# Kernel tuning notes

Hardware: AMD Instinct MI355X
Metric: run time of the kernel (lower is better)

Reference implementation:

```python
import jax, jax.numpy as jnp
import numpy as np


def setup_inputs() -> dict:
    key = jax.random.key(0)
    k1, k2 = jax.random.split(key)
    B, C, H, W = 4, 64, 256, 512
    l_fmap = jax.random.normal(k1, (B, C, H, W), dtype=jnp.float32)
    r_fmap = jax.random.normal(k2, (B, C, H, W), dtype=jnp.float32)
    return {"l_fmap": l_fmap, "r_fmap": r_fmap, "max_disp": 48}


def reference(l_fmap, r_fmap, max_disp):
    # l_fmap, r_fmap: [B, C, H, W]
    w = l_fmap.shape[-1]
    # zero-pad right fmap along width by max_disp on both sides
    r_pad = jnp.pad(r_fmap, ((0, 0), (0, 0), (0, 0), (max_disp, max_disp)))
    planes = []
    for d in range(-max_disp, max_disp + 1):  # fixed small loop over 2*max_disp+1 disparities
        begin = max_disp - d
        # channel-mean of elementwise correlation at shift d -> [B, H, W]
        planes.append(jnp.mean(l_fmap * r_pad[:, :, :, begin:begin + w], axis=1))
    # cost volume: [B, 2*max_disp+1, H, W]
    return jnp.stack(planes, axis=1)
```

## Files before the change

kernel.cpp:

```cpp
#include <hip/hip_runtime.h>


#define B_  4
#define C_  64
#define H_  256
#define W_  512
#define ND  97
#define HW  (H_ * W_)

#define WBLK 256
#define RCOL 352
#define PADH 257
#define CH0  49

typedef __attribute__((ext_vector_type(8))) short  short8;
typedef __attribute__((ext_vector_type(4))) float  floatx4;

__device__ __forceinline__ unsigned f2bf(float f) {
    unsigned u = __builtin_bit_cast(unsigned, f);
    return (u + 0x7FFFu + ((u >> 16) & 1u)) >> 16;
}

union SM {
    struct {
        short l[WBLK * C_];
        short r[RCOL * C_];
    } st;
    float out_s[CH0 * PADH];
};

__global__ __launch_bounds__(512, 4) void cost_volume_kernel(
    const float* __restrict__ L, const float* __restrict__ R,
    float* __restrict__ out)
{
    __shared__ SM sm;
    const int tid  = threadIdx.x;
    const int half = blockIdx.x;
    const int h    = blockIdx.y;
    const int b    = blockIdx.z;
    const int w0   = half << 8;
    const size_t in_base = (((size_t)b * C_) * H_ + h) * (size_t)W_;

    {
        const int wl = tid & 255;
        const int ch = tid >> 8;
        const int m  = wl & 15, wq = wl >> 4;
        const float* lp = L + in_base + w0 + wl;
        const float* rp = R + in_base + w0 + wl;
        #pragma unroll
        for (int i = 0; i < 4; ++i) {
            const int cc = ch + 2 * i;
            unsigned dl[4], dr[4];
            #pragma unroll
            for (int jj = 0; jj < 4; ++jj) {
                float l0 = lp[(size_t)(cc * 8 + 2 * jj)     * HW] * 0.015625f;
                float l1 = lp[(size_t)(cc * 8 + 2 * jj + 1) * HW] * 0.015625f;
                float r0 = rp[(size_t)(cc * 8 + 2 * jj)     * HW];
                float r1 = rp[(size_t)(cc * 8 + 2 * jj + 1) * HW];
                dl[jj] = f2bf(l0) | (f2bf(l1) << 16);
                dr[jj] = f2bf(r0) | (f2bf(r1) << 16);
            }
            const int lchunk = ( wq      * 8 + cc) * 16 + m;
            const int rchunk = ((wq + 3) * 8 + cc) * 16 + m;
            *((uint4*)&sm.st.l[lchunk * 8]) = make_uint4(dl[0], dl[1], dl[2], dl[3]);
            *((uint4*)&sm.st.r[rchunk * 8]) = make_uint4(dr[0], dr[1], dr[2], dr[3]);
        }
    }
    if (tid < 192) {
        const int ch = tid & 1;
        const int hl = tid >> 1;
        const int ul = (hl < 48) ? hl : hl + 256;
        const int u  = w0 - 48 + ul;
        const bool valid = (unsigned)u < (unsigned)W_;
        const int m = ul & 15, uq = ul >> 4;
        const float* rp = R + in_base + (valid ? u : 0);
        #pragma unroll
        for (int i = 0; i < 4; ++i) {
            const int cc = ch + 2 * i;
            unsigned dr[4];
            #pragma unroll
            for (int jj = 0; jj < 4; ++jj) {
                float r0 = rp[(size_t)(cc * 8 + 2 * jj)     * HW];
                float r1 = rp[(size_t)(cc * 8 + 2 * jj + 1) * HW];
                r0 = valid ? r0 : 0.f;
                r1 = valid ? r1 : 0.f;
                dr[jj] = f2bf(r0) | (f2bf(r1) << 16);
            }
            const int rchunk = (uq * 8 + cc) * 16 + m;
            *((uint4*)&sm.st.r[rchunk * 8]) = make_uint4(dr[0], dr[1], dr[2], dr[3]);
        }
    }
    __syncthreads();

    const int lane = tid & 63;
    const int wv   = tid >> 6;
    const int q    = lane >> 4, m16 = lane & 15;
    const short8* lv = (const short8*)sm.st.l;
    const short8* rv = (const short8*)sm.st.r;

    floatx4 acc[2][7];
    #pragma unroll
    for (int hf = 0; hf < 2; ++hf) {
        const int lt = wv + 8 * hf;
        const short8 a0 = lv[(lt * 8 +     q) * 16 + m16];
        const short8 a1 = lv[(lt * 8 + 4 + q) * 16 + m16];
        #pragma unroll
        for (int t = 0; t < 7; ++t) {
            const int ut = lt + t;
            floatx4 c = {0.f, 0.f, 0.f, 0.f};
            const short8 b0 = rv[(ut * 8 +     q) * 16 + m16];
            const short8 b1 = rv[(ut * 8 + 4 + q) * 16 + m16];
            c = __builtin_amdgcn_mfma_f32_16x16x32_bf16(a0, b0, c, 0, 0, 0);
            c = __builtin_amdgcn_mfma_f32_16x16x32_bf16(a1, b1, c, 0, 0, 0);
            acc[hf][t] = c;
        }
    }

    float* ob = out + (((size_t)b * ND) * H_ + h) * (size_t)W_ + w0;
    int lo = 0;
    #pragma unroll
    for (int ck = 0; ck < 2; ++ck) {
        const int cnt = ck ? (ND - CH0) : CH0;
        __syncthreads();
        #pragma unroll
        for (int hf = 0; hf < 2; ++hf) {
            const int lt = wv + 8 * hf;
            #pragma unroll
            for (int t = 0; t < 7; ++t) {
                #pragma unroll
                for (int r = 0; r < 4; ++r) {
                    const int ml    = q * 4 + r;
                    const int d_idx = ml - m16 + 96 - 16 * t;
                    const int drel  = d_idx - lo;
                    if ((unsigned)drel < (unsigned)cnt)
                        sm.out_s[drel * PADH + lt * 16 + ml] = acc[hf][t][r];
                }
            }
        }
        __syncthreads();
        for (int i = tid; i < cnt * WBLK; i += 512) {
            const int pr = i >> 8, w = i & 255;
            ob[(size_t)(lo + pr) * HW + w] = sm.out_s[pr * PADH + w];
        }
        lo += CH0;
    }
}

extern "C" void kernel_launch(void* const* d_in, const int* in_sizes, int n_in,
                              void* d_out, int out_size, void* d_ws, size_t ws_size,
                              hipStream_t stream) {
    const float* L = (const float*)d_in[0];
    const float* R = (const float*)d_in[1];
    float* out = (float*)d_out;
    (void)in_sizes; (void)n_in; (void)d_ws; (void)ws_size; (void)out_size;
    dim3 grid(2, H_, B_);
    hipLaunchKernelGGL(cost_volume_kernel, grid, dim3(512), 0, stream, L, R, out);
}
```

Before: 394.2 us.

## Make cost-volume kernel persistent with register-prefetched next-row loads

```diff
diff --git a/kernel.cpp b/kernel.cpp
--- a/kernel.cpp
+++ b/kernel.cpp
@@ -12,6 +12,8 @@
 #define RCOL 352
 #define PADH 257
 #define CH0  49
+#define NBLK 256
+#define NROW 8
 
 typedef __attribute__((ext_vector_type(8))) short  short8;
 typedef __attribute__((ext_vector_type(4))) float  floatx4;
@@ -21,128 +23,159 @@
     return (u + 0x7FFFu + ((u >> 16) & 1u)) >> 16;
 }
 
-union SM {
-    struct {
-        short l[WBLK * C_];
-        short r[RCOL * C_];
-    } st;
+struct SM {
+    short l[WBLK * C_];
+    short r[RCOL * C_];
     float out_s[CH0 * PADH];
 };
 
-__global__ __launch_bounds__(512, 4) void cost_volume_kernel(
+__global__ __launch_bounds__(512, 2) void cost_volume_kernel(
     const float* __restrict__ L, const float* __restrict__ R,
     float* __restrict__ out)
 {
     __shared__ SM sm;
     const int tid  = threadIdx.x;
-    const int half = blockIdx.x;
-    const int h    = blockIdx.y;
-    const int b    = blockIdx.z;
+    const int bid  = blockIdx.x;
+    const int half = bid & 1;
+    const int hb   = bid >> 1;
     const int w0   = half << 8;
-    const size_t in_base = (((size_t)b * C_) * H_ + h) * (size_t)W_;
 
-    {
-        const int wl = tid & 255;
-        const int ch = tid >> 8;
-        const int m  = wl & 15, wq = wl >> 4;
-        const float* lp = L + in_base + w0 + wl;
-        const float* rp = R + in_base + w0 + wl;
+    const int wl = tid & 255;
+    const int ch = tid >> 8;
+    const int m  = wl & 15, wq = wl >> 4;
+
+    const bool hhalo = tid < 384;
+    const int hcol = tid % 96;
+    const int hch  = tid / 96;
+    const int hul  = (hcol < 48) ? hcol : hcol + 256;
+    const int hu   = w0 - 48 + hul;
+    const bool hvalid = hhalo && ((unsigned)hu < (unsigned)W_);
+
+    float Lf[32], Rf[32], Hf[16];
+
+    auto issue = [&](int k) {
+        const int b = k >> 1;
+        const int h = hb + ((k & 1) << 7);
+        const size_t base = ((size_t)b * C_ * H_ + h) * (size_t)W_;
+        const float* lp = L + base + w0 + wl;
+        const float* rp = R + base + w0 + wl;
+        #pragma unroll
+        for (int i = 0; i < 4; ++i) {
+            const int cc = ch + 2 * i;
+            #pragma unroll
+            for (int jj = 0; jj < 8; ++jj) {
+                Lf[i * 8 + jj] = lp[(size_t)(cc * 8 + jj) * HW];
+                Rf[i * 8 + jj] = rp[(size_t)(cc * 8 + jj) * HW];
+            }
+        }
+        if (hhalo) {
+            const float* hp = R + base + (hvalid ? hu : (w0 + wl));
+            #pragma unroll
+            for (int kk = 0; kk < 16; ++kk)
+                Hf[kk] = hp[(size_t)(hch * 16 + kk) * HW];
+        }
+    };
+
+    auto commit = [&]() {
         #pragma unroll
         for (int i = 0; i < 4; ++i) {
             const int cc = ch + 2 * i;
             unsigned dl[4], dr[4];
             #pragma unroll
             for (int jj = 0; jj < 4; ++jj) {
-                float l0 = lp[(size_t)(cc * 8 + 2 * jj)     * HW] * 0.015625f;
-                float l1 = lp[(size_t)(cc * 8 + 2 * jj + 1) * HW] * 0.015625f;
-                float r0 = rp[(size_t)(cc * 8 + 2 * jj)     * HW];
-                float r1 = rp[(size_t)(cc * 8 + 2 * jj + 1) * HW];
-                dl[jj] = f2bf(l0) | (f2bf(l1) << 16);
-                dr[jj] = f2bf(r0) | (f2bf(r1) << 16);
+                dl[jj] = f2bf(Lf[i * 8 + 2 * jj]     * 0.015625f)
+                       | (f2bf(Lf[i * 8 + 2 * jj + 1] * 0.015625f) << 16);
+                dr[jj] = f2bf(Rf[i * 8 + 2 * jj])
+                       | (f2bf(Rf[i * 8 + 2 * jj + 1]) << 16);
             }
-            const int lchunk = ( wq      * 8 + cc) * 16 + m;
-            const int rchunk = ((wq + 3) * 8 + cc) * 16 + m;
-            *((uint4*)&sm.st.l[lchunk * 8]) = make_uint4(dl[0], dl[1], dl[2], dl[3]);
-            *((uint4*)&sm.st.r[rchunk * 8]) = make_uint4(dr[0], dr[1], dr[2], dr[3]);
+            *((uint4*)&sm.l[(( wq      * 8 + cc) * 16 + m) * 8]) =
+                make_uint4(dl[0], dl[1], dl[2], dl[3]);
+            *((uint4*)&sm.r[(((wq + 3) * 8 + cc) * 16 + m) * 8]) =
+                make_uint4(dr[0], dr[1], dr[2], dr[3]);
         }
-    }
-    if (tid < 192) {
-        const int ch = tid & 1;
-        const int hl = tid >> 1;
-        const int ul = (hl < 48) ? hl : hl + 256;
-        const int u  = w0 - 48 + ul;
-        const bool valid = (unsigned)u < (unsigned)W_;
-        const int m = ul & 15, uq = ul >> 4;
-        const float* rp = R + in_base + (valid ? u : 0);
-        #pragma unroll
-        for (int i = 0; i < 4; ++i) {
-            const int cc = ch + 2 * i;
-            unsigned dr[4];
+        if (hhalo) {
+            const int hm = hul & 15, huq = hul >> 4;
             #pragma unroll
-            for (int jj = 0; jj < 4; ++jj) {
-                float r0 = rp[(size_t)(cc * 8 + 2 * jj)     * HW];
-                float r1 = rp[(size_t)(cc * 8 + 2 * jj + 1) * HW];
-                r0 = valid ? r0 : 0.f;
-                r1 = valid ? r1 : 0.f;
-                dr[jj] = f2bf(r0) | (f2bf(r1) << 16);
+            for (int t2 = 0; t2 < 2; ++t2) {
+                const int cc = 2 * hch + t2;
+                unsigned dr[4];
+                #pragma unroll
+                for (int jj = 0; jj < 4; ++jj) {
+                    float r0 = hvalid ? Hf[t2 * 8 + 2 * jj]     : 0.f;
+                    float r1 = hvalid ? Hf[t2 * 8 + 2 * jj + 1] : 0.f;
+                    dr[jj] = f2bf(r0) | (f2bf(r1) << 16);
+                }
+                *((uint4*)&sm.r[((huq * 8 + cc) * 16 + hm) * 8]) =
+                    make_uint4(dr[0], dr[1], dr[2], dr[3]);
             }
-            const int rchunk = (uq * 8 + cc) * 16 + m;
-            *((uint4*)&sm.st.r[rchunk * 8]) = make_uint4(dr[0], dr[1], dr[2], dr[3]);
         }
-    }
-    __syncthreads();
+    };
 
     const int lane = tid & 63;
     const int wv   = tid >> 6;
     const int q    = lane >> 4, m16 = lane & 15;
-    const short8* lv = (const short8*)sm.st.l;
-    const short8* rv = (const short8*)sm.st.r;
+    const short8* lv = (const short8*)sm.l;
+    const short8* rv = (const short8*)sm.r;
 
-    floatx4 acc[2][7];
-    #pragma unroll
-    for (int hf = 0; hf < 2; ++hf) {
-        const int lt = wv + 8 * hf;
-        const short8 a0 = lv[(lt * 8 +     q) * 16 + m16];
-        const short8 a1 = lv[(lt * 8 + 4 + q) * 16 + m16];
-        #pragma unroll
-        for (int t = 0; t < 7; ++t) {
-            const int ut = lt + t;
-            floatx4 c = {0.f, 0.f, 0.f, 0.f};
-            const short8 b0 = rv[(ut * 8 +     q) * 16 + m16];
-            const short8 b1 = rv[(ut * 8 + 4 + q) * 16 + m16];
-            c = __builtin_amdgcn_mfma_f32_16x16x32_bf16(a0, b0, c, 0, 0, 0);
-            c = __builtin_amdgcn_mfma_f32_16x16x32_bf16(a1, b1, c, 0, 0, 0);
-            acc[hf][t] = c;
-        }
-    }
+    issue(0);
+    commit();
+    __syncthreads();
 
-    float* ob = out + (((size_t)b * ND) * H_ + h) * (size_t)W_ + w0;
-    int lo = 0;
-    #pragma unroll
-    for (int ck = 0; ck < 2; ++ck) {
-        const int cnt = ck ? (ND - CH0) : CH0;
-        __syncthreads();
+    for (int k = 0; k < NROW; ++k) {
+        const int b = k >> 1;
+        const int h = hb + ((k & 1) << 7);
+        float* ob = out + ((size_t)b * ND * H_ + h) * (size_t)W_ + w0;
+
+        floatx4 acc[2][7];
         #pragma unroll
         for (int hf = 0; hf < 2; ++hf) {
             const int lt = wv + 8 * hf;
+            const short8 a0 = lv[(lt * 8 +     q) * 16 + m16];
+            const short8 a1 = lv[(lt * 8 + 4 + q) * 16 + m16];
             #pragma unroll
             for (int t = 0; t < 7; ++t) {
+                const int ut = lt + t;
+                floatx4 c = {0.f, 0.f, 0.f, 0.f};
+                const short8 b0 = rv[(ut * 8 +     q) * 16 + m16];
+                const short8 b1 = rv[(ut * 8 + 4 + q) * 16 + m16];
+                c = __builtin_amdgcn_mfma_f32_16x16x32_bf16(a0, b0, c, 0, 0, 0);
+                c = __builtin_amdgcn_mfma_f32_16x16x32_bf16(a1, b1, c, 0, 0, 0);
+                acc[hf][t] = c;
+            }
+        }
+
+        if (k + 1 < NROW) issue(k + 1);
+
+        int lo = 0;
+        #pragma unroll
+        for (int ck = 0; ck < 2; ++ck) {
+            const int cnt = ck ? (ND - CH0) : CH0;
+            if (ck) __syncthreads();
+            #pragma unroll
+            for (int hf = 0; hf < 2; ++hf) {
+                const int lt = wv + 8 * hf;
                 #pragma unroll
-                for (int r = 0; r < 4; ++r) {
-                    const int ml    = q * 4 + r;
-                    const int d_idx = ml - m16 + 96 - 16 * t;
-                    const int drel  = d_idx - lo;
-                    if ((unsigned)drel < (unsigned)cnt)
-                        sm.out_s[drel * PADH + lt * 16 + ml] = acc[hf][t][r];
+                for (int t = 0; t < 7; ++t) {
+                    #pragma unroll
+                    for (int r = 0; r < 4; ++r) {
+                        const int ml    = q * 4 + r;
+                        const int d_idx = ml - m16 + 96 - 16 * t;
+                        const int drel  = d_idx - lo;
+                        if ((unsigned)drel < (unsigned)cnt)
+                            sm.out_s[drel * PADH + lt * 16 + ml] = acc[hf][t][r];
+                    }
                 }
             }
+            __syncthreads();
+            for (int i = tid; i < cnt * WBLK; i += 512) {
+                const int pr = i >> 8, w = i & 255;
+                ob[(size_t)(lo + pr) * HW + w] = sm.out_s[pr * PADH + w];
+            }
+            lo += CH0;
         }
+
+        if (k + 1 < NROW) commit();
         __syncthreads();
-        for (int i = tid; i < cnt * WBLK; i += 512) {
-            const int pr = i >> 8, w = i & 255;
-            ob[(size_t)(lo + pr) * HW + w] = sm.out_s[pr * PADH + w];
-        }
-        lo += CH0;
     }
 }
 
@@ -153,6 +186,6 @@
     const float* R = (const float*)d_in[1];
     float* out = (float*)d_out;
     (void)in_sizes; (void)n_in; (void)d_ws; (void)ws_size; (void)out_size;
-    dim3 grid(2, H_, B_);
+    dim3 grid(NBLK);
     hipLaunchKernelGGL(cost_volume_kernel, grid, dim3(512), 0, stream, L, R, out);
 }
```

New measurement: 389.5 us. About the same (-1.2%).
